# Performance work log

Hardware: AMD Instinct MI355X
Metric: run time of the kernel (lower is better)

The kernel has to match this reference:

```python
import jax, jax.numpy as jnp
import numpy as np

MAX_DELTAS = 4  # number of concurrently loaded delta adapters


def _dequant(qw, qz, sc):
    """GPTQ-style 4-bit dequant with a single group (g_idx == 0).

    qw: [D, O, K//8] int32, 8 x 4-bit values packed along the input (K) dim.
    qz: [D, O//8, 1] int32, 8 x 4-bit zero points packed along the output dim.
    sc: [D, O, 1] float scales (one group).
    Returns dense delta weights [D, O, K].
    """
    shifts = jnp.arange(8, dtype=jnp.int32) * 4
    D, O, Kp = qw.shape
    w = ((qw[:, :, :, None] >> shifts) & 0xF).reshape(D, O, Kp * 8)   # [D,O,K]
    z = ((qz[:, :, 0][:, :, None] >> shifts) & 0xF).reshape(D, O)     # [D,O]
    return (w.astype(sc.dtype) - (z.astype(sc.dtype) + 1.0)[:, :, None]) * sc


def setup_inputs() -> dict:
    key = jax.random.key(0)
    ks = jax.random.split(key, 16)
    T, IN = 1024, 4096
    Q, KV = 4096, 1024  # 32 q-heads, 8 kv-heads, head_size 128
    OUT = Q + 2 * KV    # 6144
    D, PACK = MAX_DELTAS, 8
    IMAX = np.int32(2**31 - 1)
    return {
        "x": jax.random.normal(ks[0], (T, IN), dtype=jnp.float32),
        "w_base": jax.random.normal(ks[1], (OUT, IN), dtype=jnp.float32) * 0.02,
        "bias": jax.random.normal(ks[2], (OUT,), dtype=jnp.float32) * 0.02,
        "qweight_q": jax.random.randint(ks[3], (D, Q, IN // PACK), 0, IMAX, dtype=jnp.int32),
        "qweight_k": jax.random.randint(ks[4], (D, KV, IN // PACK), 0, IMAX, dtype=jnp.int32),
        "qweight_v": jax.random.randint(ks[5], (D, KV, IN // PACK), 0, IMAX, dtype=jnp.int32),
        "qzeros_q": jax.random.randint(ks[6], (D, Q // PACK, 1), 0, IMAX, dtype=jnp.int32),
        "qzeros_k": jax.random.randint(ks[7], (D, KV // PACK, 1), 0, IMAX, dtype=jnp.int32),
        "qzeros_v": jax.random.randint(ks[8], (D, KV // PACK, 1), 0, IMAX, dtype=jnp.int32),
        "scales_q": jax.random.uniform(ks[9], (D, Q, 1), dtype=jnp.float32) * 0.01,
        "scales_k": jax.random.uniform(ks[10], (D, KV, 1), dtype=jnp.float32) * 0.01,
        "scales_v": jax.random.uniform(ks[11], (D, KV, 1), dtype=jnp.float32) * 0.01,
        "indices": jax.random.randint(ks[12], (T,), 0, D, dtype=jnp.int32),
    }


def reference(x, w_base, bias, qweight_q, qweight_k, qweight_v,
              qzeros_q, qzeros_k, qzeros_v, scales_q, scales_k, scales_v,
              indices):
    # Base fused QKV projection.
    out = x @ w_base.T + bias  # [T, OUT]
    # Dequantize the three packed delta stacks and concatenate along out dim,
    # matching the (q, k, v) output_slices scatter of apply_delta.
    Wd = jnp.concatenate([
        _dequant(qweight_q, qzeros_q, scales_q),
        _dequant(qweight_k, qzeros_k, scales_k),
        _dequant(qweight_v, qzeros_v, scales_v),
    ], axis=1)  # [D, OUT, IN]
    # Per-token indexed delta matmul: token t uses adapter indices[t].
    for d in range(MAX_DELTAS):
        xm = jnp.where((indices == d)[:, None], x, 0.0)  # [T, IN]
        out = out + xm @ Wd[d].T
    return out
```

## Files before the change

kernel.cpp:

```cpp
#include <hip/hip_runtime.h>
#include <stdint.h>

#define T_TOK 1024
#define K_IN  4096
#define N_OUT 6144
#define N_Q   4096
#define N_KV  1024
#define N_D   4
#define KP    512

#define TM 128
#define TN 128
#define BK 64
#define PM_MAX 1536
#define MT (PM_MAX/TM)
#define NT (N_OUT/TN)

typedef __attribute__((ext_vector_type(8)))  short  short8;
typedef __attribute__((ext_vector_type(4)))  float  float4v;

__device__ __forceinline__ ushort f2bf(float f) {
    uint32_t u = __float_as_uint(f);
    u = (u + 0x7FFFu + ((u >> 16) & 1u)) >> 16;
    return (ushort)u;
}
__device__ __forceinline__ uint pack2(ushort a, ushort b) {
    return (uint)a | ((uint)b << 16);
}

__global__ void build_perm_kernel(const int* __restrict__ indices,
                                  int* __restrict__ perm,
                                  int* __restrict__ pofs) {
    __shared__ int cnt[N_D], cur[N_D], ps[N_D + 1];
    int tid = threadIdx.x;
    if (tid < N_D) { cnt[tid] = 0; cur[tid] = 0; }
    __syncthreads();
    for (int t = tid; t < T_TOK; t += blockDim.x) atomicAdd(&cnt[indices[t]], 1);
    for (int p = tid; p < PM_MAX; p += blockDim.x) perm[p] = -1;
    __syncthreads();
    if (tid == 0) {
        int run = 0;
        for (int d = 0; d < N_D; d++) { ps[d] = run; run += ((cnt[d] + TM - 1) / TM) * TM; }
        ps[N_D] = run;
        for (int d = 0; d <= N_D; d++) pofs[d] = ps[d];
    }
    __syncthreads();
    for (int t = tid; t < T_TOK; t += blockDim.x) {
        int d = indices[t];
        int r = atomicAdd(&cur[d], 1);
        perm[ps[d] + r] = t;
    }
}

__global__ void dequant_wall_kernel(const float* __restrict__ w_base,
                                    const int* __restrict__ qw_q, const int* __restrict__ qw_k, const int* __restrict__ qw_v,
                                    const int* __restrict__ qz_q, const int* __restrict__ qz_k, const int* __restrict__ qz_v,
                                    const float* __restrict__ sc_q, const float* __restrict__ sc_k, const float* __restrict__ sc_v,
                                    ushort* __restrict__ wall) {
    int id  = blockIdx.x * blockDim.x + threadIdx.x;
    int kq  = id & (KP - 1);
    int oid = id >> 9;
    int o   = oid % N_OUT;
    int d   = oid / N_OUT;

    const int* qw; const int* qz; const float* sc; int r, Osec;
    if (o < N_Q)            { qw = qw_q; qz = qz_q; sc = sc_q; r = o;                Osec = N_Q;  }
    else if (o < N_Q + N_KV){ qw = qw_k; qz = qz_k; sc = sc_k; r = o - N_Q;          Osec = N_KV; }
    else                    { qw = qw_v; qz = qz_v; sc = sc_v; r = o - (N_Q + N_KV); Osec = N_KV; }

    int   q  = qw[((size_t)d * Osec + r) * KP + kq];
    int   zq = qz[(size_t)d * (Osec / 8) + (r >> 3)];
    float s  = sc[(size_t)d * Osec + r];
    float zs = (float)(((zq >> ((r & 7) * 4)) & 0xF) + 1) * s;

    const float* wb = w_base + (size_t)o * K_IN + (size_t)kq * 8;
    ushort res[8];
#pragma unroll
    for (int j = 0; j < 8; j++) {
        float v = wb[j] + (float)((q >> (4 * j)) & 0xF) * s - zs;
        res[j] = f2bf(v);
    }
    uint4 packv;
    packv.x = pack2(res[0], res[1]); packv.y = pack2(res[2], res[3]);
    packv.z = pack2(res[4], res[5]); packv.w = pack2(res[6], res[7]);
    *(uint4*)(wall + ((size_t)d * N_OUT + o) * K_IN + (size_t)kq * 8) = packv;
}

__global__ void build_xp_kernel(const float* __restrict__ x,
                                const int* __restrict__ perm,
                                ushort* __restrict__ xp) {
    int pm = blockIdx.x;
    int c0 = blockIdx.y * 2048 + threadIdx.x * 8;
    int tok = perm[pm];
    ushort res[8];
    if (tok < 0) {
#pragma unroll
        for (int j = 0; j < 8; j++) res[j] = 0;
    } else {
        const float* src = x + (size_t)tok * K_IN + c0;
#pragma unroll
        for (int j = 0; j < 8; j++) res[j] = f2bf(src[j]);
    }
    uint4 packv;
    packv.x = pack2(res[0], res[1]); packv.y = pack2(res[2], res[3]);
    packv.z = pack2(res[4], res[5]); packv.w = pack2(res[6], res[7]);
    *(uint4*)(xp + (size_t)pm * K_IN + c0) = packv;
}

__global__ __launch_bounds__(256, 2) void gemm_kernel(
    const ushort* __restrict__ xp, const ushort* __restrict__ wall,
    const int* __restrict__ perm, const int* __restrict__ pofs,
    const float* __restrict__ bias, float* __restrict__ out) {

    __shared__ ushort As[TM * BK];
    __shared__ ushort Bs[TN * BK];

    int bn = blockIdx.x, bm = blockIdx.y;
    int m0 = bm * TM, n0 = bn * TN;
    int ptot = pofs[N_D];
    if (m0 >= ptot) return;
    int d = 0;
    while (d < N_D - 1 && m0 >= pofs[d + 1]) d++;

    const ushort* wsec = wall + (size_t)d * N_OUT * K_IN;

    int tid  = threadIdx.x;
    int lane = tid & 63;
    int wv   = tid >> 6;
    int wm   = (wv & 1) * 64;
    int wn   = (wv >> 1) * 64;
    int quad = lane >> 4;
    int l16  = lane & 15;

    const float4v zero4 = {0.f, 0.f, 0.f, 0.f};
    float4v acc[4][4];
#pragma unroll
    for (int i = 0; i < 4; i++)
#pragma unroll
        for (int j = 0; j < 4; j++) acc[i][j] = zero4;

    for (int k0 = 0; k0 < K_IN; k0 += BK) {
#pragma unroll
        for (int w = 0; w < 4; w++) {
            int c   = w * 256 + tid;
            int row = c >> 3, ck = c & 7;
            const ushort* ga = xp   + (size_t)(m0 + row) * K_IN + k0 + ck * 8;
            const ushort* gb = wsec + (size_t)(n0 + row) * K_IN + k0 + ck * 8;
            int base = (w * 256 + (tid & ~63)) * 8;
            __builtin_amdgcn_global_load_lds((const __attribute__((address_space(1))) void*)ga,
                                             (__attribute__((address_space(3))) void*)(As + base), 16, 0, 0);
            __builtin_amdgcn_global_load_lds((const __attribute__((address_space(1))) void*)gb,
                                             (__attribute__((address_space(3))) void*)(Bs + base), 16, 0, 0);
        }
        __syncthreads();

#pragma unroll
        for (int kk = 0; kk < BK; kk += 32) {
            short8 a[4], b[4];
#pragma unroll
            for (int i = 0; i < 4; i++)
                a[i] = *(const short8*)(As + (wm + i * 16 + l16) * BK + kk + quad * 8);
#pragma unroll
            for (int j = 0; j < 4; j++)
                b[j] = *(const short8*)(Bs + (wn + j * 16 + l16) * BK + kk + quad * 8);
#pragma unroll
            for (int i = 0; i < 4; i++)
#pragma unroll
                for (int j = 0; j < 4; j++)
                    acc[i][j] = __builtin_amdgcn_mfma_f32_16x16x32_bf16(a[i], b[j], acc[i][j], 0, 0, 0);
        }
        __syncthreads();
    }

#pragma unroll
    for (int i = 0; i < 4; i++) {
        int toks[4];
#pragma unroll
        for (int r = 0; r < 4; r++) toks[r] = perm[m0 + wm + i * 16 + quad * 4 + r];
#pragma unroll
        for (int j = 0; j < 4; j++) {
            int col = n0 + wn + j * 16 + l16;
            float bv = bias[col];
#pragma unroll
            for (int r = 0; r < 4; r++) {
                int tok = toks[r];
                if (tok >= 0) out[(size_t)tok * N_OUT + col] = acc[i][j][r] + bv;
            }
        }
    }
}

extern "C" void kernel_launch(void* const* d_in, const int* in_sizes, int n_in,
                              void* d_out, int out_size, void* d_ws, size_t ws_size,
                              hipStream_t stream) {
    const float* x      = (const float*)d_in[0];
    const float* w_base = (const float*)d_in[1];
    const float* bias   = (const float*)d_in[2];
    const int*   qw_q   = (const int*)d_in[3];
    const int*   qw_k   = (const int*)d_in[4];
    const int*   qw_v   = (const int*)d_in[5];
    const int*   qz_q   = (const int*)d_in[6];
    const int*   qz_k   = (const int*)d_in[7];
    const int*   qz_v   = (const int*)d_in[8];
    const float* sc_q   = (const float*)d_in[9];
    const float* sc_k   = (const float*)d_in[10];
    const float* sc_v   = (const float*)d_in[11];
    const int*   indices= (const int*)d_in[12];
    float* out = (float*)d_out;

    char* ws = (char*)d_ws;
    ushort* wall = (ushort*)ws;
    size_t wall_bytes = (size_t)N_D * N_OUT * K_IN * 2;
    ushort* xp = (ushort*)(ws + wall_bytes);
    size_t xp_bytes = (size_t)PM_MAX * K_IN * 2;
    int* perm = (int*)(ws + wall_bytes + xp_bytes);
    int* pofs = perm + PM_MAX;

    build_perm_kernel<<<1, 256, 0, stream>>>(indices, perm, pofs);
    dequant_wall_kernel<<<(N_D * N_OUT * KP) / 256, 256, 0, stream>>>(
        w_base, qw_q, qw_k, qw_v, qz_q, qz_k, qz_v, sc_q, sc_k, sc_v, wall);
    build_xp_kernel<<<dim3(PM_MAX, 2), 256, 0, stream>>>(x, perm, xp);
    gemm_kernel<<<dim3(NT, MT), 256, 0, stream>>>(xp, wall, perm, pofs, bias, out);
}
```

Before: 406.4 us.

## Split-K GEMM with atomic epilogue, XOR-swizzled LDS, and shared w_base dequant loop

The GEMM is split along K into two halves over a third grid dimension, and partial sums are combined with float atomicAdd into an output that a new kernel first fills with the bias. LDS tiles use an XOR swizzle on the 16-byte chunk index to cut bank conflicts, and launch bounds rise to 4 waves per SIMD. The dequant kernel now loads each w_base element once with float4 loads and loops over the four deltas, which cuts redundant reads of w_base. The cost is atomic traffic, a full output initialisation pass, non-deterministic summation order, and possible register spilling under the tighter occupancy bound.

Measured after the change: 376.9 us. 7.2% less time.

```diff
diff --git a/kernel.cpp b/kernel.cpp
--- a/kernel.cpp
+++ b/kernel.cpp
@@ -12,6 +12,8 @@
 #define TM 128
 #define TN 128
 #define BK 64
+#define KSPLIT 2
+#define KHALF (K_IN / KSPLIT)
 #define PM_MAX 1536
 #define MT (PM_MAX/TM)
 #define NT (N_OUT/TN)
@@ -59,31 +61,36 @@
                                     ushort* __restrict__ wall) {
     int id  = blockIdx.x * blockDim.x + threadIdx.x;
     int kq  = id & (KP - 1);
-    int oid = id >> 9;
-    int o   = oid % N_OUT;
-    int d   = oid / N_OUT;
+    int o   = id >> 9;
 
     const int* qw; const int* qz; const float* sc; int r, Osec;
     if (o < N_Q)            { qw = qw_q; qz = qz_q; sc = sc_q; r = o;                Osec = N_Q;  }
     else if (o < N_Q + N_KV){ qw = qw_k; qz = qz_k; sc = sc_k; r = o - N_Q;          Osec = N_KV; }
     else                    { qw = qw_v; qz = qz_v; sc = sc_v; r = o - (N_Q + N_KV); Osec = N_KV; }
 
-    int   q  = qw[((size_t)d * Osec + r) * KP + kq];
-    int   zq = qz[(size_t)d * (Osec / 8) + (r >> 3)];
-    float s  = sc[(size_t)d * Osec + r];
-    float zs = (float)(((zq >> ((r & 7) * 4)) & 0xF) + 1) * s;
-
-    const float* wb = w_base + (size_t)o * K_IN + (size_t)kq * 8;
-    ushort res[8];
-#pragma unroll
-    for (int j = 0; j < 8; j++) {
-        float v = wb[j] + (float)((q >> (4 * j)) & 0xF) * s - zs;
-        res[j] = f2bf(v);
-    }
-    uint4 packv;
-    packv.x = pack2(res[0], res[1]); packv.y = pack2(res[2], res[3]);
-    packv.z = pack2(res[4], res[5]); packv.w = pack2(res[6], res[7]);
-    *(uint4*)(wall + ((size_t)d * N_OUT + o) * K_IN + (size_t)kq * 8) = packv;
+    const float* wbp = w_base + (size_t)o * K_IN + (size_t)kq * 8;
+    float4 wb0 = *(const float4*)(wbp);
+    float4 wb1 = *(const float4*)(wbp + 4);
+    float wb[8] = {wb0.x, wb0.y, wb0.z, wb0.w, wb1.x, wb1.y, wb1.z, wb1.w};
+
+#pragma unroll
+    for (int d = 0; d < N_D; d++) {
+        int   q  = qw[((size_t)d * Osec + r) * KP + kq];
+        int   zq = qz[(size_t)d * (Osec / 8) + (r >> 3)];
+        float s  = sc[(size_t)d * Osec + r];
+        float zs = (float)(((zq >> ((r & 7) * 4)) & 0xF) + 1) * s;
+
+        ushort res[8];
+#pragma unroll
+        for (int j = 0; j < 8; j++) {
+            float v = wb[j] + (float)((q >> (4 * j)) & 0xF) * s - zs;
+            res[j] = f2bf(v);
+        }
+        uint4 packv;
+        packv.x = pack2(res[0], res[1]); packv.y = pack2(res[2], res[3]);
+        packv.z = pack2(res[4], res[5]); packv.w = pack2(res[6], res[7]);
+        *(uint4*)(wall + ((size_t)d * N_OUT + o) * K_IN + (size_t)kq * 8) = packv;
+    }
 }
 
 __global__ void build_xp_kernel(const float* __restrict__ x,
@@ -107,15 +114,24 @@
     *(uint4*)(xp + (size_t)pm * K_IN + c0) = packv;
 }
 
-__global__ __launch_bounds__(256, 2) void gemm_kernel(
+__global__ void init_out_kernel(const float* __restrict__ bias,
+                                float* __restrict__ out) {
+    int id = blockIdx.x * blockDim.x + threadIdx.x;
+    int n4 = id & (N_OUT / 4 - 1);
+    int t  = id / (N_OUT / 4);
+    float4 b = *(const float4*)(bias + n4 * 4);
+    *(float4*)(out + (size_t)t * N_OUT + n4 * 4) = b;
+}
+
+__global__ __launch_bounds__(256, 4) void gemm_kernel(
     const ushort* __restrict__ xp, const ushort* __restrict__ wall,
     const int* __restrict__ perm, const int* __restrict__ pofs,
-    const float* __restrict__ bias, float* __restrict__ out) {
+    float* __restrict__ out) {
 
     __shared__ ushort As[TM * BK];
     __shared__ ushort Bs[TN * BK];
 
-    int bn = blockIdx.x, bm = blockIdx.y;
+    int bn = blockIdx.x, bm = blockIdx.y, kz = blockIdx.z;
     int m0 = bm * TM, n0 = bn * TN;
     int ptot = pofs[N_D];
     if (m0 >= ptot) return;
@@ -131,6 +147,7 @@
     int wn   = (wv >> 1) * 64;
     int quad = lane >> 4;
     int l16  = lane & 15;
+    int xa   = l16 & 7;
 
     const float4v zero4 = {0.f, 0.f, 0.f, 0.f};
     float4v acc[4][4];
@@ -139,13 +156,15 @@
 #pragma unroll
         for (int j = 0; j < 4; j++) acc[i][j] = zero4;
 
-    for (int k0 = 0; k0 < K_IN; k0 += BK) {
+    int kbase = kz * KHALF;
+    for (int k0 = kbase; k0 < kbase + KHALF; k0 += BK) {
 #pragma unroll
         for (int w = 0; w < 4; w++) {
-            int c   = w * 256 + tid;
-            int row = c >> 3, ck = c & 7;
-            const ushort* ga = xp   + (size_t)(m0 + row) * K_IN + k0 + ck * 8;
-            const ushort* gb = wsec + (size_t)(n0 + row) * K_IN + k0 + ck * 8;
+            int p   = w * 256 + tid;
+            int row = p >> 3;
+            int ckl = (p & 7) ^ (row & 7);
+            const ushort* ga = xp   + (size_t)(m0 + row) * K_IN + k0 + ckl * 8;
+            const ushort* gb = wsec + (size_t)(n0 + row) * K_IN + k0 + ckl * 8;
             int base = (w * 256 + (tid & ~63)) * 8;
             __builtin_amdgcn_global_load_lds((const __attribute__((address_space(1))) void*)ga,
                                              (__attribute__((address_space(3))) void*)(As + base), 16, 0, 0);
@@ -156,13 +175,14 @@
 
 #pragma unroll
         for (int kk = 0; kk < BK; kk += 32) {
+            int ckb = (kk >> 3) + quad;
             short8 a[4], b[4];
 #pragma unroll
             for (int i = 0; i < 4; i++)
-                a[i] = *(const short8*)(As + (wm + i * 16 + l16) * BK + kk + quad * 8);
+                a[i] = *(const short8*)(As + (wm + i * 16 + l16) * BK + (ckb ^ xa) * 8);
 #pragma unroll
             for (int j = 0; j < 4; j++)
-                b[j] = *(const short8*)(Bs + (wn + j * 16 + l16) * BK + kk + quad * 8);
+                b[j] = *(const short8*)(Bs + (wn + j * 16 + l16) * BK + (ckb ^ xa) * 8);
 #pragma unroll
             for (int i = 0; i < 4; i++)
 #pragma unroll
@@ -180,11 +200,10 @@
 #pragma unroll
         for (int j = 0; j < 4; j++) {
             int col = n0 + wn + j * 16 + l16;
-            float bv = bias[col];
 #pragma unroll
             for (int r = 0; r < 4; r++) {
                 int tok = toks[r];
-                if (tok >= 0) out[(size_t)tok * N_OUT + col] = acc[i][j][r] + bv;
+                if (tok >= 0) atomicAdd(out + (size_t)tok * N_OUT + col, acc[i][j][r]);
             }
         }
     }
@@ -217,8 +236,9 @@
     int* pofs = perm + PM_MAX;
 
     build_perm_kernel<<<1, 256, 0, stream>>>(indices, perm, pofs);
-    dequant_wall_kernel<<<(N_D * N_OUT * KP) / 256, 256, 0, stream>>>(
+    dequant_wall_kernel<<<(N_OUT * KP) / 256, 256, 0, stream>>>(
         w_base, qw_q, qw_k, qw_v, qz_q, qz_k, qz_v, sc_q, sc_k, sc_v, wall);
     build_xp_kernel<<<dim3(PM_MAX, 2), 256, 0, stream>>>(x, perm, xp);
-    gemm_kernel<<<dim3(NT, MT), 256, 0, stream>>>(xp, wall, perm, pofs, bias, out);
-}
+    init_out_kernel<<<(T_TOK * N_OUT / 4) / 256, 256, 0, stream>>>(bias, out);
+    gemm_kernel<<<dim3(NT, MT, KSPLIT), 256, 0, stream>>>(xp, wall, perm, pofs, out);
+}
```
